# Kernel optimization log

Hardware: AMD Instinct MI355X
Metric: run time of the kernel (lower is better)

## Reference

```python
import jax, jax.numpy as jnp
import numpy as np

CHUNK_SIZE = 2048
EPS = 1e-12  # torch F.normalize clamps the norm at 1e-12


def _l2_normalize(x, axis):
    n = jnp.sqrt(jnp.sum(x * x, axis=axis, keepdims=True))
    return x / jnp.maximum(n, EPS)


def _nnfm_loss(F_r, F_s, chunk_size=CHUNK_SIZE):
    B, C, H_r, W_r = F_r.shape
    _, _, H_s, W_s = F_s.shape
    N_r = H_r * W_r
    N_s = H_s * W_s
    assert N_r % chunk_size == 0, "N_r must be divisible by chunk_size for this reference"
    n_chunks = N_r // chunk_size

    F_s_norm = _l2_normalize(F_s.reshape(B, C, N_s), axis=1)  # (B, C, N_s)
    F_r_flat = F_r.reshape(B, C, N_r)
    # (n_chunks, B, C, chunk) -- contiguous chunks along N_r, matching the torch loop
    chunks = F_r_flat.reshape(B, C, n_chunks, chunk_size).transpose(2, 0, 1, 3)

    def body(chunk):  # chunk: (B, C, chunk_size)
        cn = _l2_normalize(chunk, axis=1)
        sim = jnp.einsum('bcn,bcm->bnm', cn, F_s_norm)  # (B, chunk, N_s)
        # min(1 - sim) over N_s == 1 - max(sim)
        return 1.0 - jnp.max(sim, axis=2)  # (B, chunk)

    min_dists = jax.lax.map(body, chunks)  # (n_chunks, B, chunk) -- bounded memory
    return jnp.mean(min_dists)


def setup_inputs() -> dict:
    key = jax.random.key(0)
    k1, k2 = jax.random.split(key)
    F_r = jax.random.normal(k1, (1, 768, 128, 128), dtype=jnp.float32)
    F_s = jax.random.normal(k2, (1, 768, 128, 128), dtype=jnp.float32)
    return {"F_r": F_r, "F_s": F_s}


def reference(F_r, F_s):
    return _nnfm_loss(F_r, F_s)
```

## Files before the change

kernel.cpp:

```cpp
#include <hip/hip_runtime.h>
#include <cstdint>
#include <cstddef>

#define C_DIM 768
#define N_DIM 16384

typedef __attribute__((ext_vector_type(8))) short short8;
typedef __attribute__((ext_vector_type(4))) float f32x4;

__device__ __forceinline__ ushort f2bf(float f) {
    uint32_t u = __float_as_uint(f);
    uint32_t r = 0x7fffu + ((u >> 16) & 1u);
    return (ushort)((u + r) >> 16);
}

__device__ __forceinline__ void async_ld16(const void* g, void* l) {
    __builtin_amdgcn_global_load_lds(
        (__attribute__((address_space(1))) void*)g,
        (__attribute__((address_space(3))) void*)l,
        16, 0, 0);
}

__global__ __launch_bounds__(256) void norm_tr(const float* __restrict__ F0,
                                               ushort* __restrict__ T0,
                                               const float* __restrict__ F1,
                                               ushort* __restrict__ T1) {
    const float*  F = blockIdx.y ? F1 : F0;
    ushort*       T = blockIdx.y ? T1 : T0;
    const int i0 = blockIdx.x * 64;
    const int t  = threadIdx.x;
    const int tx = t & 63;
    const int ty = t >> 6;

    float ss = 0.f;
    for (int c = ty; c < C_DIM; c += 4) {
        float v = F[(size_t)c * N_DIM + i0 + tx];
        ss += v * v;
    }
    __shared__ float red[4][64];
    __shared__ float scale[64];
    red[ty][tx] = ss;
    __syncthreads();
    if (t < 64) {
        float s = red[0][t] + red[1][t] + red[2][t] + red[3][t];
        float n = sqrtf(s);
        scale[t] = 1.0f / fmaxf(n, 1e-12f);
    }
    __syncthreads();

    __shared__ float tile[64][65];
    const int i_l   = t >> 3;
    const int c_off = (t & 7) * 8;
    for (int c0 = 0; c0 < C_DIM; c0 += 64) {
        #pragma unroll
        for (int rr = 0; rr < 16; ++rr) {
            int c_l = rr * 4 + ty;
            tile[c_l][tx] = F[(size_t)(c0 + c_l) * N_DIM + i0 + tx] * scale[tx];
        }
        __syncthreads();
        #pragma unroll
        for (int half = 0; half < 2; ++half) {
            int il = i_l + half * 32;
            __align__(16) ushort pack[8];
            #pragma unroll
            for (int j = 0; j < 8; ++j)
                pack[j] = f2bf(tile[c_off + j][il]);
            *(uint4*)&T[(size_t)(i0 + il) * C_DIM + c0 + c_off] = *(const uint4*)pack;
        }
        __syncthreads();
    }
}

__global__ __launch_bounds__(256) void gemm_rowmax(const ushort* __restrict__ A,
                                                   const ushort* __restrict__ B,
                                                   unsigned* __restrict__ rowkey) {
    __shared__ __align__(16) ushort As[128 * 32];
    __shared__ __align__(16) ushort Bs[128 * 32];

    const int t    = threadIdx.x;
    const int lane = t & 63;
    const int w    = t >> 6;
    const int wm   = w >> 1, wn = w & 1;
    const int m0   = blockIdx.y * 128;
    const int n0   = blockIdx.x * 128;

    f32x4 acc[4][4];
    #pragma unroll
    for (int i = 0; i < 4; ++i)
        #pragma unroll
        for (int j = 0; j < 4; ++j)
            acc[i][j] = (f32x4){0.f, 0.f, 0.f, 0.f};

    const int r  = t >> 2;
    const int kl = (t & 3) ^ ((t >> 3) & 3);
    const int kq = kl * 8;
    const ushort* ag0 = A + (size_t)(m0 + r) * C_DIM + kq;
    const ushort* ag1 = ag0 + (size_t)64 * C_DIM;
    const ushort* bg0 = B + (size_t)(n0 + r) * C_DIM + kq;
    const ushort* bg1 = bg0 + (size_t)64 * C_DIM;
    ushort* asd0 = As + t * 8;
    ushort* asd1 = As + 64 * 32 + t * 8;
    ushort* bsd0 = Bs + t * 8;
    ushort* bsd1 = Bs + 64 * 32 + t * 8;

    const int qp    = ((lane >> 4) ^ ((lane >> 1) & 3)) * 8;
    const int a_off = (wm * 64 + (lane & 15)) * 32 + qp;
    const int b_off = (wn * 64 + (lane & 15)) * 32 + qp;

    for (int k0 = 0; k0 < C_DIM; k0 += 32) {
        async_ld16(ag0 + k0, asd0);
        async_ld16(ag1 + k0, asd1);
        async_ld16(bg0 + k0, bsd0);
        async_ld16(bg1 + k0, bsd1);
        __syncthreads();

        short8 af[4], bfr[4];
        #pragma unroll
        for (int mt = 0; mt < 4; ++mt)
            af[mt] = *(const short8*)(As + a_off + mt * 16 * 32);
        #pragma unroll
        for (int nt = 0; nt < 4; ++nt)
            bfr[nt] = *(const short8*)(Bs + b_off + nt * 16 * 32);
        #pragma unroll
        for (int mt = 0; mt < 4; ++mt)
            #pragma unroll
            for (int nt = 0; nt < 4; ++nt)
                acc[mt][nt] = __builtin_amdgcn_mfma_f32_16x16x32_bf16(
                    af[mt], bfr[nt], acc[mt][nt], 0, 0, 0);
        __syncthreads();
    }

    #pragma unroll
    for (int mt = 0; mt < 4; ++mt) {
        #pragma unroll
        for (int reg = 0; reg < 4; ++reg) {
            float v = fmaxf(fmaxf(acc[mt][0][reg], acc[mt][1][reg]),
                            fmaxf(acc[mt][2][reg], acc[mt][3][reg]));
            #pragma unroll
            for (int off = 1; off < 16; off <<= 1)
                v = fmaxf(v, __shfl_xor(v, off, 64));
            if ((lane & 15) == 0) {
                int m = m0 + wm * 64 + mt * 16 + (lane >> 4) * 4 + reg;
                unsigned u = __float_as_uint(v);
                u = (u & 0x80000000u) ? ~u : (u | 0x80000000u);
                atomicMax(&rowkey[m], u);
            }
        }
    }
}

__global__ __launch_bounds__(1024) void finalize(const unsigned* __restrict__ rowkey,
                                                 float* __restrict__ out) {
    const int t = threadIdx.x;
    float s = 0.f;
    for (int i = t; i < N_DIM; i += 1024) {
        unsigned u = rowkey[i];
        float f = (u & 0x80000000u) ? __uint_as_float(u ^ 0x80000000u)
                                    : __uint_as_float(~u);
        s += f;
    }
    #pragma unroll
    for (int off = 32; off >= 1; off >>= 1)
        s += __shfl_down(s, off, 64);
    __shared__ float part[16];
    if ((t & 63) == 0) part[t >> 6] = s;
    __syncthreads();
    if (t == 0) {
        float tot = 0.f;
        #pragma unroll
        for (int i = 0; i < 16; ++i) tot += part[i];
        out[0] = 1.0f - tot * (1.0f / (float)N_DIM);
    }
}

extern "C" void kernel_launch(void* const* d_in, const int* in_sizes, int n_in,
                              void* d_out, int out_size, void* d_ws, size_t ws_size,
                              hipStream_t stream) {
    const float* F_r = (const float*)d_in[0];
    const float* F_s = (const float*)d_in[1];

    ushort*   Rt     = (ushort*)d_ws;
    ushort*   St     = Rt + (size_t)N_DIM * C_DIM;
    unsigned* rowkey = (unsigned*)(St + (size_t)N_DIM * C_DIM);
    float*    out    = (float*)d_out;

    hipLaunchKernelGGL(norm_tr, dim3(N_DIM / 64, 2), dim3(256), 0, stream,
                       F_r, Rt, F_s, St);
    hipMemsetAsync(rowkey, 0, N_DIM * sizeof(unsigned), stream);
    hipLaunchKernelGGL(gemm_rowmax, dim3(N_DIM / 128, N_DIM / 128), dim3(256),
                       0, stream, Rt, St, rowkey);
    hipLaunchKernelGGL(finalize, dim3(1), dim3(1024), 0, stream, rowkey, out);
}
```

Baseline: 787.4 us.

## Switch GEMM from bf16 to fp8 with scaled 32x32x64 MFMA

The normalize-transpose pass now scales the unit vectors by 16 and packs them to fp8 instead of bf16. The GEMM reads fp8 tiles 64 wide in k and uses the MX-scaled 32x32x64 f8f6f4 MFMA. Its scale exponent 0x7B (2^-4 per operand) undoes the factor of 16. This halves the bytes in the workspace and the LDS traffic and doubles the MFMA throughput per instruction. The cost is a much coarser similarity value, which can change which candidate wins the max and so shift the loss beyond bf16 accuracy.

After: 1.430 ms. 1.82x slower.

```diff
diff --git a/kernel.cpp b/kernel.cpp
--- a/kernel.cpp
+++ b/kernel.cpp
@@ -5,14 +5,9 @@
 #define C_DIM 768
 #define N_DIM 16384
 
-typedef __attribute__((ext_vector_type(8))) short short8;
-typedef __attribute__((ext_vector_type(4))) float f32x4;
-
-__device__ __forceinline__ ushort f2bf(float f) {
-    uint32_t u = __float_as_uint(f);
-    uint32_t r = 0x7fffu + ((u >> 16) & 1u);
-    return (ushort)((u + r) >> 16);
-}
+typedef __attribute__((ext_vector_type(8)))  int   i32x8;
+typedef __attribute__((ext_vector_type(4)))  int   i32x4;
+typedef __attribute__((ext_vector_type(16))) float f32x16;
 
 __device__ __forceinline__ void async_ld16(const void* g, void* l) {
     __builtin_amdgcn_global_load_lds(
@@ -22,11 +17,11 @@
 }
 
 __global__ __launch_bounds__(256) void norm_tr(const float* __restrict__ F0,
-                                               ushort* __restrict__ T0,
+                                               unsigned char* __restrict__ T0,
                                                const float* __restrict__ F1,
-                                               ushort* __restrict__ T1) {
-    const float*  F = blockIdx.y ? F1 : F0;
-    ushort*       T = blockIdx.y ? T1 : T0;
+                                               unsigned char* __restrict__ T1) {
+    const float*   F = blockIdx.y ? F1 : F0;
+    unsigned char* T = blockIdx.y ? T1 : T0;
     const int i0 = blockIdx.x * 64;
     const int t  = threadIdx.x;
     const int tx = t & 63;
@@ -44,7 +39,7 @@
     if (t < 64) {
         float s = red[0][t] + red[1][t] + red[2][t] + red[3][t];
         float n = sqrtf(s);
-        scale[t] = 1.0f / fmaxf(n, 1e-12f);
+        scale[t] = 16.0f / fmaxf(n, 1e-12f);
     }
     __syncthreads();
 
@@ -61,21 +56,25 @@
         #pragma unroll
         for (int half = 0; half < 2; ++half) {
             int il = i_l + half * 32;
-            __align__(16) ushort pack[8];
-            #pragma unroll
-            for (int j = 0; j < 8; ++j)
-                pack[j] = f2bf(tile[c_off + j][il]);
-            *(uint4*)&T[(size_t)(i0 + il) * C_DIM + c0 + c_off] = *(const uint4*)pack;
-        }
-        __syncthreads();
-    }
-}
-
-__global__ __launch_bounds__(256) void gemm_rowmax(const ushort* __restrict__ A,
-                                                   const ushort* __restrict__ B,
+            float v[8];
+            #pragma unroll
+            for (int j = 0; j < 8; ++j) v[j] = tile[c_off + j][il];
+            int lo = __builtin_amdgcn_cvt_pk_fp8_f32(v[0], v[1], 0, false);
+            lo     = __builtin_amdgcn_cvt_pk_fp8_f32(v[2], v[3], lo, true);
+            int hi = __builtin_amdgcn_cvt_pk_fp8_f32(v[4], v[5], 0, false);
+            hi     = __builtin_amdgcn_cvt_pk_fp8_f32(v[6], v[7], hi, true);
+            uint2 u; u.x = (unsigned)lo; u.y = (unsigned)hi;
+            *(uint2*)&T[(size_t)(i0 + il) * C_DIM + c0 + c_off] = u;
+        }
+        __syncthreads();
+    }
+}
+
+__global__ __launch_bounds__(256) void gemm_rowmax(const unsigned char* __restrict__ A,
+                                                   const unsigned char* __restrict__ B,
                                                    unsigned* __restrict__ rowkey) {
-    __shared__ __align__(16) ushort As[128 * 32];
-    __shared__ __align__(16) ushort Bs[128 * 32];
+    __shared__ __align__(16) unsigned char As[128 * 64];
+    __shared__ __align__(16) unsigned char Bs[128 * 64];
 
     const int t    = threadIdx.x;
     const int lane = t & 63;
@@ -84,63 +83,83 @@
     const int m0   = blockIdx.y * 128;
     const int n0   = blockIdx.x * 128;
 
-    f32x4 acc[4][4];
+    f32x16 acc[2][2];
     #pragma unroll
-    for (int i = 0; i < 4; ++i)
-        #pragma unroll
-        for (int j = 0; j < 4; ++j)
-            acc[i][j] = (f32x4){0.f, 0.f, 0.f, 0.f};
-
-    const int r  = t >> 2;
-    const int kl = (t & 3) ^ ((t >> 3) & 3);
-    const int kq = kl * 8;
-    const ushort* ag0 = A + (size_t)(m0 + r) * C_DIM + kq;
-    const ushort* ag1 = ag0 + (size_t)64 * C_DIM;
-    const ushort* bg0 = B + (size_t)(n0 + r) * C_DIM + kq;
-    const ushort* bg1 = bg0 + (size_t)64 * C_DIM;
-    ushort* asd0 = As + t * 8;
-    ushort* asd1 = As + 64 * 32 + t * 8;
-    ushort* bsd0 = Bs + t * 8;
-    ushort* bsd1 = Bs + 64 * 32 + t * 8;
-
-    const int qp    = ((lane >> 4) ^ ((lane >> 1) & 3)) * 8;
-    const int a_off = (wm * 64 + (lane & 15)) * 32 + qp;
-    const int b_off = (wn * 64 + (lane & 15)) * 32 + qp;
-
-    for (int k0 = 0; k0 < C_DIM; k0 += 32) {
+    for (int i = 0; i < 2; ++i)
+        #pragma unroll
+        for (int j = 0; j < 2; ++j)
+            #pragma unroll
+            for (int e = 0; e < 16; ++e)
+                acc[i][j][e] = 0.f;
+
+    const int r    = t >> 2;
+    const int clog = (t & 3) ^ ((t >> 3) & 3);
+    const unsigned char* ag0 = A + (size_t)(m0 + r) * C_DIM + clog * 16;
+    const unsigned char* ag1 = ag0 + (size_t)64 * C_DIM;
+    const unsigned char* bg0 = B + (size_t)(n0 + r) * C_DIM + clog * 16;
+    const unsigned char* bg1 = bg0 + (size_t)64 * C_DIM;
+    unsigned char* asd0 = As + t * 16;
+    unsigned char* asd1 = As + 4096 + t * 16;
+    unsigned char* bsd0 = Bs + t * 16;
+    unsigned char* bsd1 = Bs + 4096 + t * 16;
+
+    const int row = lane & 31;
+    const int j   = lane >> 5;
+    const int f   = (row >> 1) & 3;
+    const int bp  = j ^ (f >> 1);
+    const int lo_off = bp * 32 + (f & 1) * 16;
+    const int hi_off = bp * 32 + ((f & 1) ^ 1) * 16;
+    const int a_base0 = (wm * 64 +      row) * 64;
+    const int a_base1 = (wm * 64 + 32 + row) * 64;
+    const int b_base0 = (wn * 64 +      row) * 64;
+    const int b_base1 = (wn * 64 + 32 + row) * 64;
+
+    for (int k0 = 0; k0 < C_DIM; k0 += 64) {
         async_ld16(ag0 + k0, asd0);
         async_ld16(ag1 + k0, asd1);
         async_ld16(bg0 + k0, bsd0);
         async_ld16(bg1 + k0, bsd1);
         __syncthreads();
 
-        short8 af[4], bfr[4];
-        #pragma unroll
-        for (int mt = 0; mt < 4; ++mt)
-            af[mt] = *(const short8*)(As + a_off + mt * 16 * 32);
-        #pragma unroll
-        for (int nt = 0; nt < 4; ++nt)
-            bfr[nt] = *(const short8*)(Bs + b_off + nt * 16 * 32);
-        #pragma unroll
-        for (int mt = 0; mt < 4; ++mt)
-            #pragma unroll
-            for (int nt = 0; nt < 4; ++nt)
-                acc[mt][nt] = __builtin_amdgcn_mfma_f32_16x16x32_bf16(
-                    af[mt], bfr[nt], acc[mt][nt], 0, 0, 0);
+        i32x8 af[2], bf[2];
+        {
+            i32x4 lo, hi;
+            lo = *(const i32x4*)(As + a_base0 + lo_off);
+            hi = *(const i32x4*)(As + a_base0 + hi_off);
+            af[0] = (i32x8){lo.x, lo.y, lo.z, lo.w, hi.x, hi.y, hi.z, hi.w};
+            lo = *(const i32x4*)(As + a_base1 + lo_off);
+            hi = *(const i32x4*)(As + a_base1 + hi_off);
+            af[1] = (i32x8){lo.x, lo.y, lo.z, lo.w, hi.x, hi.y, hi.z, hi.w};
+            lo = *(const i32x4*)(Bs + b_base0 + lo_off);
+            hi = *(const i32x4*)(Bs + b_base0 + hi_off);
+            bf[0] = (i32x8){lo.x, lo.y, lo.z, lo.w, hi.x, hi.y, hi.z, hi.w};
+            lo = *(const i32x4*)(Bs + b_base1 + lo_off);
+            hi = *(const i32x4*)(Bs + b_base1 + hi_off);
+            bf[1] = (i32x8){lo.x, lo.y, lo.z, lo.w, hi.x, hi.y, hi.z, hi.w};
+        }
+        #pragma unroll
+        for (int mi = 0; mi < 2; ++mi)
+            #pragma unroll
+            for (int ni = 0; ni < 2; ++ni)
+                acc[mi][ni] = __builtin_amdgcn_mfma_scale_f32_32x32x64_f8f6f4(
+                    af[mi], bf[ni], acc[mi][ni],
+                    0, 0,
+                    0, 0x7B7B7B7B,
+                    0, 0x7B7B7B7B);
         __syncthreads();
     }
 
     #pragma unroll
-    for (int mt = 0; mt < 4; ++mt) {
-        #pragma unroll
-        for (int reg = 0; reg < 4; ++reg) {
-            float v = fmaxf(fmaxf(acc[mt][0][reg], acc[mt][1][reg]),
-                            fmaxf(acc[mt][2][reg], acc[mt][3][reg]));
-            #pragma unroll
-            for (int off = 1; off < 16; off <<= 1)
+    for (int mi = 0; mi < 2; ++mi) {
+        #pragma unroll
+        for (int reg = 0; reg < 16; ++reg) {
+            float v = fmaxf(acc[mi][0][reg], acc[mi][1][reg]);
+            #pragma unroll
+            for (int off = 1; off < 32; off <<= 1)
                 v = fmaxf(v, __shfl_xor(v, off, 64));
-            if ((lane & 15) == 0) {
-                int m = m0 + wm * 64 + mt * 16 + (lane >> 4) * 4 + reg;
+            if ((lane & 31) == 0) {
+                int m = m0 + wm * 64 + mi * 32 + (reg & 3) + 8 * (reg >> 2)
+                        + 4 * (lane >> 5);
                 unsigned u = __float_as_uint(v);
                 u = (u & 0x80000000u) ? ~u : (u | 0x80000000u);
                 atomicMax(&rowkey[m], u);
@@ -179,10 +198,10 @@
     const float* F_r = (const float*)d_in[0];
     const float* F_s = (const float*)d_in[1];
 
-    ushort*   Rt     = (ushort*)d_ws;
-    ushort*   St     = Rt + (size_t)N_DIM * C_DIM;
-    unsigned* rowkey = (unsigned*)(St + (size_t)N_DIM * C_DIM);
-    float*    out    = (float*)d_out;
+    unsigned char* Rt = (unsigned char*)d_ws;
+    unsigned char* St = Rt + (size_t)N_DIM * C_DIM;
+    unsigned* rowkey  = (unsigned*)(St + (size_t)N_DIM * C_DIM);
+    float*    out     = (float*)d_out;
 
     hipLaunchKernelGGL(norm_tr, dim3(N_DIM / 64, 2), dim3(256), 0, stream,
                        F_r, Rt, F_s, St);
```

## Double-buffer GEMM LDS tiles and remap blocks per XCD for L2 locality

Applied to the files above, without the earlier changes.

The GEMM main loop now uses two LDS buffers for the A and B tiles. The next K-slice is prefetched with async global-to-LDS loads while MFMAs run on the current slice, and the second barrier per iteration is removed. The 2D grid is flattened to 1D and blockIdx is remapped so that each XCD handles a contiguous group of N-tile columns, aiming to improve L2 reuse of B tiles. This doubles LDS use per block, which may reduce occupancy.

New measurement: 692.9 us. 12.0% less time.

```diff
diff --git a/kernel.cpp b/kernel.cpp
--- a/kernel.cpp
+++ b/kernel.cpp
@@ -74,15 +74,21 @@
 __global__ __launch_bounds__(256) void gemm_rowmax(const ushort* __restrict__ A,
                                                    const ushort* __restrict__ B,
                                                    unsigned* __restrict__ rowkey) {
-    __shared__ __align__(16) ushort As[128 * 32];
-    __shared__ __align__(16) ushort Bs[128 * 32];
+    __shared__ __align__(16) ushort As[2][128 * 32];
+    __shared__ __align__(16) ushort Bs[2][128 * 32];
 
     const int t    = threadIdx.x;
     const int lane = t & 63;
     const int w    = t >> 6;
     const int wm   = w >> 1, wn = w & 1;
-    const int m0   = blockIdx.y * 128;
-    const int n0   = blockIdx.x * 128;
+
+    const int bid   = blockIdx.x;
+    const int xcd   = bid & 7;
+    const int local = bid >> 3;
+    const int half_ = local >> 10;
+    const int rem   = local & 1023;
+    const int m0    = (rem >> 3) * 128;
+    const int n0    = (xcd * 16 + half_ * 8 + (rem & 7)) * 128;
 
     f32x4 acc[4][4];
     #pragma unroll
@@ -92,42 +98,49 @@
             acc[i][j] = (f32x4){0.f, 0.f, 0.f, 0.f};
 
     const int r  = t >> 2;
-    const int kl = (t & 3) ^ ((t >> 3) & 3);
-    const int kq = kl * 8;
+    const int kq = ((t & 3) ^ ((t >> 3) & 3)) * 8;
     const ushort* ag0 = A + (size_t)(m0 + r) * C_DIM + kq;
     const ushort* ag1 = ag0 + (size_t)64 * C_DIM;
     const ushort* bg0 = B + (size_t)(n0 + r) * C_DIM + kq;
     const ushort* bg1 = bg0 + (size_t)64 * C_DIM;
-    ushort* asd0 = As + t * 8;
-    ushort* asd1 = As + 64 * 32 + t * 8;
-    ushort* bsd0 = Bs + t * 8;
-    ushort* bsd1 = Bs + 64 * 32 + t * 8;
+    const int ld0 = t * 8, ld1 = 64 * 32 + t * 8;
 
     const int qp    = ((lane >> 4) ^ ((lane >> 1) & 3)) * 8;
     const int a_off = (wm * 64 + (lane & 15)) * 32 + qp;
     const int b_off = (wn * 64 + (lane & 15)) * 32 + qp;
 
+    async_ld16(ag0, As[0] + ld0);
+    async_ld16(ag1, As[0] + ld1);
+    async_ld16(bg0, Bs[0] + ld0);
+    async_ld16(bg1, Bs[0] + ld1);
+
+    int buf = 0;
     for (int k0 = 0; k0 < C_DIM; k0 += 32) {
-        async_ld16(ag0 + k0, asd0);
-        async_ld16(ag1 + k0, asd1);
-        async_ld16(bg0 + k0, bsd0);
-        async_ld16(bg1 + k0, bsd1);
         __syncthreads();
-
+        if (k0 + 32 < C_DIM) {
+            const int kn = k0 + 32, nb = buf ^ 1;
+            async_ld16(ag0 + kn, As[nb] + ld0);
+            async_ld16(ag1 + kn, As[nb] + ld1);
+            async_ld16(bg0 + kn, Bs[nb] + ld0);
+            async_ld16(bg1 + kn, Bs[nb] + ld1);
+        }
+
+        const ushort* Ab = As[buf];
+        const ushort* Bb = Bs[buf];
         short8 af[4], bfr[4];
         #pragma unroll
         for (int mt = 0; mt < 4; ++mt)
-            af[mt] = *(const short8*)(As + a_off + mt * 16 * 32);
+            af[mt] = *(const short8*)(Ab + a_off + mt * 16 * 32);
         #pragma unroll
         for (int nt = 0; nt < 4; ++nt)
-            bfr[nt] = *(const short8*)(Bs + b_off + nt * 16 * 32);
+            bfr[nt] = *(const short8*)(Bb + b_off + nt * 16 * 32);
         #pragma unroll
         for (int mt = 0; mt < 4; ++mt)
             #pragma unroll
             for (int nt = 0; nt < 4; ++nt)
                 acc[mt][nt] = __builtin_amdgcn_mfma_f32_16x16x32_bf16(
                     af[mt], bfr[nt], acc[mt][nt], 0, 0, 0);
-        __syncthreads();
+        buf ^= 1;
     }
 
     #pragma unroll
@@ -187,7 +200,7 @@
     hipLaunchKernelGGL(norm_tr, dim3(N_DIM / 64, 2), dim3(256), 0, stream,
                        F_r, Rt, F_s, St);
     hipMemsetAsync(rowkey, 0, N_DIM * sizeof(unsigned), stream);
-    hipLaunchKernelGGL(gemm_rowmax, dim3(N_DIM / 128, N_DIM / 128), dim3(256),
+    hipLaunchKernelGGL(gemm_rowmax, dim3(N_DIM / 128 * N_DIM / 128), dim3(256),
                        0, stream, Rt, St, rowkey);
     hipLaunchKernelGGL(finalize, dim3(1), dim3(1024), 0, stream, rowkey, out);
 }
```
